# Kernel tuning notes

Hardware: AMD Instinct MI355X
Metric: run time of the kernel (lower is better)

Reference implementation:

```python
import jax, jax.numpy as jnp
from jax import lax
import numpy as np

NUM_LABELS = 48
BATCH, SEQ_LEN = 512, 1024


def setup_inputs() -> dict:
    key = jax.random.key(0)
    k1, k2, k3, k4, k5 = jax.random.split(key, 5)
    emissions = jax.random.normal(k1, (BATCH, SEQ_LEN, NUM_LABELS), dtype=jnp.float32)
    labels = jax.random.randint(k2, (BATCH, SEQ_LEN), 0, NUM_LABELS, dtype=jnp.int32)
    mask = jnp.ones((BATCH, SEQ_LEN), dtype=jnp.int32)
    transitions = jax.random.normal(k3, (NUM_LABELS, NUM_LABELS), dtype=jnp.float32)
    start_transitions = jax.random.normal(k4, (NUM_LABELS,), dtype=jnp.float32)
    end_transitions = jax.random.normal(k5, (NUM_LABELS,), dtype=jnp.float32)
    return {
        "emissions": emissions,
        "labels": labels,
        "mask": mask,
        "transitions": transitions,
        "start_transitions": start_transitions,
        "end_transitions": end_transitions,
    }


def _gold_score(emissions, labels, mask, transitions, start_transitions, end_transitions):
    maskf = mask.astype(emissions.dtype)
    # emissions gathered at gold labels: (B, T)
    emit = jnp.take_along_axis(emissions, labels[..., None], axis=2)[..., 0]
    # NOTE: original indexes transitions[labels_t, labels_{t-1}] (cur, prev)
    trans = transitions[labels[:, 1:], labels[:, :-1]]  # (B, T-1)
    lengths = jnp.sum(mask, axis=1) - 1  # index of last real token
    last_labels = jnp.take_along_axis(labels, lengths[:, None], axis=1)[:, 0]
    score = (start_transitions[labels[:, 0]] + emit[:, 0]
             + jnp.sum((emit[:, 1:] + trans) * maskf[:, 1:], axis=1)
             + end_transitions[last_labels])
    return score  # (B,)


def _forward_algorithm(emissions, mask, transitions, start_transitions, end_transitions):
    # carry: alpha scores (B, L)
    score0 = start_transitions[None, :] + emissions[:, 0]

    def step(score, xs):
        emit_t, mask_t = xs  # (B, L), (B,)
        # logsumexp over previous label i of score[b,i] + transitions[i,j]
        next_score = jax.nn.logsumexp(score[:, :, None] + transitions[None, :, :], axis=1) + emit_t
        score = jnp.where(mask_t[:, None].astype(bool), next_score, score)
        return score, None

    xs = (jnp.moveaxis(emissions[:, 1:], 1, 0), jnp.moveaxis(mask[:, 1:], 1, 0))
    score, _ = lax.scan(step, score0, xs)
    return jax.nn.logsumexp(score + end_transitions[None, :], axis=1)  # (B,)


def reference(emissions, labels, mask, transitions, start_transitions, end_transitions):
    gold = _gold_score(emissions, labels, mask, transitions, start_transitions, end_transitions)
    fwd = _forward_algorithm(emissions, mask, transitions, start_transitions, end_transitions)
    return jnp.mean(fwd - gold)
```

## Files before the change

kernel.cpp:

```cpp
#include <hip/hip_runtime.h>

constexpr int NL    = 48;
constexpr int SEQ   = 1024;
constexpr int BATCH = 512;

typedef float f2 __attribute__((ext_vector_type(2)));
typedef float f4 __attribute__((ext_vector_type(4)));

__device__ __forceinline__ f2 fma2(f2 a, f2 b, f2 c) {
    return __builtin_elementwise_fma(a, b, c);
}

#define CRF_STEP(T_, SLOT_, RN_) do {                                         \
    float ee_ = __expf(embuf[SLOT_]);                                         \
    int   mt_ = (int)((mb_cur >> (SLOT_)) & 1);                               \
    int   tn_ = (T_) + 8; if (tn_ > SEQ - 1) tn_ = SEQ - 1;                   \
    embuf[SLOT_] = em[tn_ * NL + jc];                                         \
    float rm_ = 1.0f;                                                         \
    if (RN_) {                                                                \
        float m_ = v;                                                         \
        _Pragma("unroll")                                                     \
        for (int o_ = 32; o_; o_ >>= 1) m_ = fmaxf(m_, __shfl_xor(m_, o_));   \
        rm_ = __builtin_amdgcn_rcpf(m_);                                      \
        S += __logf(m_);                                                      \
    }                                                                         \
    f2 c0_ = {0.f, 0.f}, c1_ = {0.f, 0.f};                                    \
    f2 c2_ = {0.f, 0.f}, c3_ = {0.f, 0.f};                                    \
    _Pragma("unroll")                                                         \
    for (int g_ = 0; g_ < 12; g_ += 2) {                                      \
        f4 s_ = svl4[g_];                                                     \
        c0_ = fma2(s_.xy, Ec2[2 * g_    ], c0_);                              \
        c1_ = fma2(s_.zw, Ec2[2 * g_ + 1], c1_);                              \
        f4 t_ = svl4[g_ + 1];                                                 \
        c2_ = fma2(t_.xy, Ec2[2 * g_ + 2], c2_);                              \
        c3_ = fma2(t_.zw, Ec2[2 * g_ + 3], c3_);                              \
    }                                                                         \
    f2 cs_ = (c0_ + c2_) + (c1_ + c3_);                                       \
    float acc_ = cs_.x + cs_.y;                                               \
    v = (mt_ ? acc_ * ee_ : v) * rm_;                                         \
    svl[tid] = v;                                                             \
} while (0)

__global__ __launch_bounds__(128)
__attribute__((amdgpu_waves_per_eu(1, 1)))
void crf_fused(
    const float* __restrict__ emissions, const int* __restrict__ labels,
    const int* __restrict__ mask, const float* __restrict__ trans,
    const float* __restrict__ startt, const float* __restrict__ endt,
    float* __restrict__ gold_out, float* __restrict__ fwd_out)
{
    const int b   = blockIdx.x;
    const int tid = threadIdx.x;
    const float* em = emissions + (size_t)b * SEQ * NL;
    const int*   mk = mask + b * SEQ;

    __shared__ alignas(16) float svl[64];

    if (tid < 64) {
        const int  j   = tid;
        const bool act = (j < NL);
        const int  jc  = act ? j : NL - 1;
        const f4*  svl4 = reinterpret_cast<const f4*>(svl);

        f2 Ec2[24];
        #pragma unroll
        for (int k = 0; k < 24; ++k) {
            f2 e_;
            e_.x = __expf(trans[(2 * k    ) * NL + jc]);
            e_.y = __expf(trans[(2 * k + 1) * NL + jc]);
            Ec2[k] = e_;
        }

        int mval = mk[tid & 7];
        unsigned long long mb_cur = __ballot(mval != 0);
        mval = mk[8 + (tid & 7)];

        float s0 = act ? (startt[jc] + em[jc]) : -3.0e38f;
        float m0 = s0;
        #pragma unroll
        for (int o = 32; o; o >>= 1) m0 = fmaxf(m0, __shfl_xor(m0, o));
        float v = act ? __expf(s0 - m0) : 0.0f;
        float S = m0;
        svl[tid] = v;

        float embuf[8];
        #pragma unroll
        for (int t = 1; t <= 8; ++t) embuf[t & 7] = em[t * NL + jc];

        CRF_STEP(1, 1, 0); CRF_STEP(2, 2, 0); CRF_STEP(3, 3, 0); CRF_STEP(4, 4, 0);
        CRF_STEP(5, 5, 1); CRF_STEP(6, 6, 0); CRF_STEP(7, 7, 0);

        for (int tb = 8; tb <= SEQ - 8; tb += 8) {
            mb_cur = __ballot(mval != 0);
            int tm = tb + 8 + (tid & 7);
            if (tm > SEQ - 1) tm = SEQ - 1;
            mval = mk[tm];
            CRF_STEP(tb + 0, 0, 1);
            CRF_STEP(tb + 1, 1, 0); CRF_STEP(tb + 2, 2, 0); CRF_STEP(tb + 3, 3, 0);
            CRF_STEP(tb + 4, 4, 1);
            CRF_STEP(tb + 5, 5, 0); CRF_STEP(tb + 6, 6, 0); CRF_STEP(tb + 7, 7, 0);
        }

        float w = act ? v * __expf(endt[jc]) : 0.0f;
        #pragma unroll
        for (int o = 32; o; o >>= 1) w += __shfl_xor(w, o);
        if (j == 0) fwd_out[b] = S + __logf(w);
    } else {
        const int l = tid - 64;
        const int* lb = labels + b * SEQ;

        float part = 0.0f; int mcnt = 0;
        for (int t = l; t < SEQ; t += 64) {
            int lt = lb[t];
            int mt = mk[t];
            mcnt += mt;
            if (t == 0) {
                part += startt[lt] + em[lt];
            } else {
                float e  = em[t * NL + lt];
                float tr = trans[lt * NL + lb[t - 1]];
                if (mt) part += e + tr;
            }
        }
        #pragma unroll
        for (int o = 32; o; o >>= 1) {
            part += __shfl_xor(part, o);
            mcnt += __shfl_xor(mcnt, o);
        }
        if (l == 0) {
            int len = mcnt - 1;
            gold_out[b] = part + endt[lb[len]];
        }
    }
}

__global__ __launch_bounds__(64) void crf_reduce(
    const float* __restrict__ gold, const float* __restrict__ fwd,
    float* __restrict__ out)
{
    const int l = threadIdx.x;
    float s = 0.0f;
    for (int bIdx = l; bIdx < BATCH; bIdx += 64) s += fwd[bIdx] - gold[bIdx];
    #pragma unroll
    for (int o = 32; o; o >>= 1) s += __shfl_xor(s, o);
    if (l == 0) out[0] = s * (1.0f / (float)BATCH);
}

extern "C" void kernel_launch(void* const* d_in, const int* in_sizes, int n_in,
                              void* d_out, int out_size, void* d_ws, size_t ws_size,
                              hipStream_t stream) {
    const float* emissions = (const float*)d_in[0];
    const int*   labels    = (const int*)d_in[1];
    const int*   mask      = (const int*)d_in[2];
    const float* trans     = (const float*)d_in[3];
    const float* startt    = (const float*)d_in[4];
    const float* endt      = (const float*)d_in[5];
    float*       out       = (float*)d_out;
    float*       wsf       = (float*)d_ws;

    crf_fused<<<BATCH, 128, 0, stream>>>(emissions, labels, mask, trans, startt, endt,
                                         wsf, wsf + BATCH);
    crf_reduce<<<1, 64, 0, stream>>>(wsf, wsf + BATCH, out);
}
```

Baseline: 324.0 us.

## Interleave two batch sequences per wave and compute renorm max from LDS

Each forward-recurrence wave now processes two batch elements in an interleaved fashion, so the independent dependency chains of two sequences can hide each other's LDS and FMA latency. Grid size is halved and each block gets two gold-score waves. The renormalisation max is now computed from the 48 values already loaded from shared memory, replacing a cross-lane shuffle reduction. The cost is doubled register pressure per wave and fewer blocks (256 on a device with many CUs), which may leave some compute units idle.

```diff
diff --git a/kernel.cpp b/kernel.cpp
--- a/kernel.cpp
+++ b/kernel.cpp
@@ -10,38 +10,51 @@
 __device__ __forceinline__ f2 fma2(f2 a, f2 b, f2 c) {
     return __builtin_elementwise_fma(a, b, c);
 }
-
-#define CRF_STEP(T_, SLOT_, RN_) do {                                         \
-    float ee_ = __expf(embuf[SLOT_]);                                         \
-    int   mt_ = (int)((mb_cur >> (SLOT_)) & 1);                               \
+__device__ __forceinline__ f2 max2(f2 a, f2 b) {
+    return __builtin_elementwise_max(a, b);
+}
+
+#define CRF_STEP(T_, SLOT_, RN_, v_, S_, eb_, mb_, em_, svl_, sv4_) do {      \
+    float ee_ = __expf(eb_[SLOT_]);                                           \
+    int   mt_ = (int)((mb_ >> (SLOT_)) & 1);                                  \
     int   tn_ = (T_) + 8; if (tn_ > SEQ - 1) tn_ = SEQ - 1;                   \
-    embuf[SLOT_] = em[tn_ * NL + jc];                                         \
-    float rm_ = 1.0f;                                                         \
-    if (RN_) {                                                                \
-        float m_ = v;                                                         \
-        _Pragma("unroll")                                                     \
-        for (int o_ = 32; o_; o_ >>= 1) m_ = fmaxf(m_, __shfl_xor(m_, o_));   \
-        rm_ = __builtin_amdgcn_rcpf(m_);                                      \
-        S += __logf(m_);                                                      \
-    }                                                                         \
+    eb_[SLOT_] = em_[tn_ * NL + jc];                                          \
+    f4 sv_[12];                                                               \
+    _Pragma("unroll")                                                         \
+    for (int g_ = 0; g_ < 12; ++g_) sv_[g_] = sv4_[g_];                       \
     f2 c0_ = {0.f, 0.f}, c1_ = {0.f, 0.f};                                    \
     f2 c2_ = {0.f, 0.f}, c3_ = {0.f, 0.f};                                    \
     _Pragma("unroll")                                                         \
     for (int g_ = 0; g_ < 12; g_ += 2) {                                      \
-        f4 s_ = svl4[g_];                                                     \
-        c0_ = fma2(s_.xy, Ec2[2 * g_    ], c0_);                              \
-        c1_ = fma2(s_.zw, Ec2[2 * g_ + 1], c1_);                              \
-        f4 t_ = svl4[g_ + 1];                                                 \
-        c2_ = fma2(t_.xy, Ec2[2 * g_ + 2], c2_);                              \
-        c3_ = fma2(t_.zw, Ec2[2 * g_ + 3], c3_);                              \
+        c0_ = fma2(sv_[g_    ].xy, Ec2[2 * g_    ], c0_);                     \
+        c1_ = fma2(sv_[g_    ].zw, Ec2[2 * g_ + 1], c1_);                     \
+        c2_ = fma2(sv_[g_ + 1].xy, Ec2[2 * g_ + 2], c2_);                     \
+        c3_ = fma2(sv_[g_ + 1].zw, Ec2[2 * g_ + 3], c3_);                     \
+    }                                                                         \
+    float rm_ = 1.0f;                                                         \
+    if (RN_) {                                                                \
+        f2 x0_ = max2(max2(sv_[0].xy,  sv_[0].zw),  max2(sv_[1].xy,  sv_[1].zw));  \
+        f2 x1_ = max2(max2(sv_[2].xy,  sv_[2].zw),  max2(sv_[3].xy,  sv_[3].zw));  \
+        f2 x2_ = max2(max2(sv_[4].xy,  sv_[4].zw),  max2(sv_[5].xy,  sv_[5].zw));  \
+        f2 x3_ = max2(max2(sv_[6].xy,  sv_[6].zw),  max2(sv_[7].xy,  sv_[7].zw));  \
+        f2 x4_ = max2(max2(sv_[8].xy,  sv_[8].zw),  max2(sv_[9].xy,  sv_[9].zw));  \
+        f2 x5_ = max2(max2(sv_[10].xy, sv_[10].zw), max2(sv_[11].xy, sv_[11].zw)); \
+        f2 y_  = max2(max2(x0_, x1_), max2(max2(x2_, x3_), max2(x4_, x5_)));  \
+        float m_ = fmaxf(y_.x, y_.y);                                         \
+        rm_ = __builtin_amdgcn_rcpf(m_);                                      \
+        S_ += __logf(m_);                                                     \
     }                                                                         \
     f2 cs_ = (c0_ + c2_) + (c1_ + c3_);                                       \
     float acc_ = cs_.x + cs_.y;                                               \
-    v = (mt_ ? acc_ * ee_ : v) * rm_;                                         \
-    svl[tid] = v;                                                             \
+    v_ = (mt_ ? acc_ * ee_ : v_) * rm_;                                       \
+    svl_[tid] = v_;                                                           \
 } while (0)
 
-__global__ __launch_bounds__(128)
+#define CRF_PAIR(T_, SLOT_, RN_)                                              \
+    CRF_STEP(T_, SLOT_, RN_, vA, SA, ebA, mbA, emA, svlA, sv4A);              \
+    CRF_STEP(T_, SLOT_, RN_, vB, SB, ebB, mbB, emB, svlB, sv4B)
+
+__global__ __launch_bounds__(192)
 __attribute__((amdgpu_waves_per_eu(1, 1)))
 void crf_fused(
     const float* __restrict__ emissions, const int* __restrict__ labels,
@@ -49,18 +62,26 @@
     const float* __restrict__ startt, const float* __restrict__ endt,
     float* __restrict__ gold_out, float* __restrict__ fwd_out)
 {
-    const int b   = blockIdx.x;
+    const int pb  = blockIdx.x;
     const int tid = threadIdx.x;
-    const float* em = emissions + (size_t)b * SEQ * NL;
-    const int*   mk = mask + b * SEQ;
-
-    __shared__ alignas(16) float svl[64];
+    const int bA  = 2 * pb;
+    const int bB  = 2 * pb + 1;
+
+    __shared__ alignas(16) float svl[2][64];
 
     if (tid < 64) {
         const int  j   = tid;
         const bool act = (j < NL);
         const int  jc  = act ? j : NL - 1;
-        const f4*  svl4 = reinterpret_cast<const f4*>(svl);
+
+        const float* emA = emissions + (size_t)bA * SEQ * NL;
+        const float* emB = emissions + (size_t)bB * SEQ * NL;
+        const int*   mkA = mask + bA * SEQ;
+        const int*   mkB = mask + bB * SEQ;
+        float* svlA = svl[0];
+        float* svlB = svl[1];
+        const f4* sv4A = reinterpret_cast<const f4*>(svlA);
+        const f4* sv4B = reinterpret_cast<const f4*>(svlB);
 
         f2 Ec2[24];
         #pragma unroll
@@ -71,53 +92,78 @@
             Ec2[k] = e_;
         }
 
-        int mval = mk[tid & 7];
-        unsigned long long mb_cur = __ballot(mval != 0);
-        mval = mk[8 + (tid & 7)];
-
-        float s0 = act ? (startt[jc] + em[jc]) : -3.0e38f;
-        float m0 = s0;
-        #pragma unroll
-        for (int o = 32; o; o >>= 1) m0 = fmaxf(m0, __shfl_xor(m0, o));
-        float v = act ? __expf(s0 - m0) : 0.0f;
-        float S = m0;
-        svl[tid] = v;
-
-        float embuf[8];
-        #pragma unroll
-        for (int t = 1; t <= 8; ++t) embuf[t & 7] = em[t * NL + jc];
-
-        CRF_STEP(1, 1, 0); CRF_STEP(2, 2, 0); CRF_STEP(3, 3, 0); CRF_STEP(4, 4, 0);
-        CRF_STEP(5, 5, 1); CRF_STEP(6, 6, 0); CRF_STEP(7, 7, 0);
+        int mvA = mkA[tid & 7];
+        int mvB = mkB[tid & 7];
+        unsigned long long mbA = __ballot(mvA != 0);
+        unsigned long long mbB = __ballot(mvB != 0);
+        mvA = mkA[8 + (tid & 7)];
+        mvB = mkB[8 + (tid & 7)];
+
+        float s0A = act ? (startt[jc] + emA[jc]) : -3.0e38f;
+        float s0B = act ? (startt[jc] + emB[jc]) : -3.0e38f;
+        float m0A = s0A, m0B = s0B;
+        #pragma unroll
+        for (int o = 32; o; o >>= 1) {
+            m0A = fmaxf(m0A, __shfl_xor(m0A, o));
+            m0B = fmaxf(m0B, __shfl_xor(m0B, o));
+        }
+        float vA = act ? __expf(s0A - m0A) : 0.0f;  float SA = m0A;
+        float vB = act ? __expf(s0B - m0B) : 0.0f;  float SB = m0B;
+        svlA[tid] = vA;
+        svlB[tid] = vB;
+
+        float ebA[8], ebB[8];
+        #pragma unroll
+        for (int t = 1; t <= 8; ++t) {
+            ebA[t & 7] = emA[t * NL + jc];
+            ebB[t & 7] = emB[t * NL + jc];
+        }
+
+        CRF_PAIR(1, 1, 0); CRF_PAIR(2, 2, 0); CRF_PAIR(3, 3, 0); CRF_PAIR(4, 4, 0);
+        CRF_PAIR(5, 5, 1); CRF_PAIR(6, 6, 0); CRF_PAIR(7, 7, 0);
 
         for (int tb = 8; tb <= SEQ - 8; tb += 8) {
-            mb_cur = __ballot(mval != 0);
+            mbA = __ballot(mvA != 0);
+            mbB = __ballot(mvB != 0);
             int tm = tb + 8 + (tid & 7);
             if (tm > SEQ - 1) tm = SEQ - 1;
-            mval = mk[tm];
-            CRF_STEP(tb + 0, 0, 1);
-            CRF_STEP(tb + 1, 1, 0); CRF_STEP(tb + 2, 2, 0); CRF_STEP(tb + 3, 3, 0);
-            CRF_STEP(tb + 4, 4, 1);
-            CRF_STEP(tb + 5, 5, 0); CRF_STEP(tb + 6, 6, 0); CRF_STEP(tb + 7, 7, 0);
-        }
-
-        float w = act ? v * __expf(endt[jc]) : 0.0f;
-        #pragma unroll
-        for (int o = 32; o; o >>= 1) w += __shfl_xor(w, o);
-        if (j == 0) fwd_out[b] = S + __logf(w);
+            mvA = mkA[tm];
+            mvB = mkB[tm];
+            CRF_PAIR(tb + 0, 0, 1);
+            CRF_PAIR(tb + 1, 1, 0); CRF_PAIR(tb + 2, 2, 0); CRF_PAIR(tb + 3, 3, 0);
+            CRF_PAIR(tb + 4, 4, 1);
+            CRF_PAIR(tb + 5, 5, 0); CRF_PAIR(tb + 6, 6, 0); CRF_PAIR(tb + 7, 7, 0);
+        }
+
+        float et = __expf(endt[jc]);
+        float wA = act ? vA * et : 0.0f;
+        float wB = act ? vB * et : 0.0f;
+        #pragma unroll
+        for (int o = 32; o; o >>= 1) {
+            wA += __shfl_xor(wA, o);
+            wB += __shfl_xor(wB, o);
+        }
+        if (j == 0) {
+            fwd_out[bA] = SA + __logf(wA);
+            fwd_out[bB] = SB + __logf(wB);
+        }
     } else {
-        const int l = tid - 64;
-        const int* lb = labels + b * SEQ;
+        const int  w   = (tid >> 6) - 1;
+        const int  l   = tid & 63;
+        const int  seq = 2 * pb + w;
+        const int* lb  = labels + seq * SEQ;
+        const int* mks = mask + seq * SEQ;
+        const float* ems = emissions + (size_t)seq * SEQ * NL;
 
         float part = 0.0f; int mcnt = 0;
         for (int t = l; t < SEQ; t += 64) {
             int lt = lb[t];
-            int mt = mk[t];
+            int mt = mks[t];
             mcnt += mt;
             if (t == 0) {
-                part += startt[lt] + em[lt];
+                part += startt[lt] + ems[lt];
             } else {
-                float e  = em[t * NL + lt];
+                float e  = ems[t * NL + lt];
                 float tr = trans[lt * NL + lb[t - 1]];
                 if (mt) part += e + tr;
             }
@@ -129,7 +175,7 @@
         }
         if (l == 0) {
             int len = mcnt - 1;
-            gold_out[b] = part + endt[lb[len]];
+            gold_out[seq] = part + endt[lb[len]];
         }
     }
 }
@@ -158,7 +204,7 @@
     float*       out       = (float*)d_out;
     float*       wsf       = (float*)d_ws;
 
-    crf_fused<<<BATCH, 128, 0, stream>>>(emissions, labels, mask, trans, startt, endt,
-                                         wsf, wsf + BATCH);
+    crf_fused<<<BATCH / 2, 192, 0, stream>>>(emissions, labels, mask, trans,
+                                             startt, endt, wsf, wsf + BATCH);
     crf_reduce<<<1, 64, 0, stream>>>(wsf, wsf + BATCH, out);
 }
```

Result: slower. 450.2 us (+39.0%).

## Replace LDS alpha broadcast with permlane swaps and DPP row rotates

Applied to the files above, without the earlier changes.

Each forward step now spreads the alpha vector across lanes with permlane32/permlane16 swaps and DPP row rotations instead of writing it to shared memory and reading it back. The transition exponentials are pre-permuted per lane to match the rotated operands. The max-renormalisation reduction also moves to DPP. This removes LDS round trips and their waits from the serial recurrence, at the cost of more cross-lane instructions and higher register pressure (64 coefficient registers).

```diff
diff --git a/kernel.cpp b/kernel.cpp
--- a/kernel.cpp
+++ b/kernel.cpp
@@ -4,41 +4,80 @@
 constexpr int SEQ   = 1024;
 constexpr int BATCH = 512;
 
-typedef float f2 __attribute__((ext_vector_type(2)));
-typedef float f4 __attribute__((ext_vector_type(4)));
-
-__device__ __forceinline__ f2 fma2(f2 a, f2 b, f2 c) {
-    return __builtin_elementwise_fma(a, b, c);
-}
+template<int N>
+__device__ __forceinline__ float rrf(float x) {
+    if constexpr (N == 0) return x;
+    else {
+        int xi = __float_as_int(x);
+        return __int_as_float(
+            __builtin_amdgcn_update_dpp(xi, xi, 0x120 | N, 0xF, 0xF, false));
+    }
+}
+template<int N>
+__device__ __forceinline__ unsigned rru(unsigned x) {
+    if constexpr (N == 0) return x;
+    else return (unsigned)
+        __builtin_amdgcn_update_dpp((int)x, (int)x, 0x120 | N, 0xF, 0xF, false);
+}
+
+__device__ __forceinline__ void spread4(unsigned x,
+        unsigned &c, unsigned &d, unsigned &e, unsigned &f) {
+    auto rA = __builtin_amdgcn_permlane32_swap(x, x, false, false);
+    auto rc = __builtin_amdgcn_permlane16_swap(rA[0], rA[0], false, false);
+    auto re = __builtin_amdgcn_permlane16_swap(rA[1], rA[1], false, false);
+    c = rc[0]; d = rc[1]; e = re[0]; f = re[1];
+}
+
+#define RF3(N_, pa_, pb_, pc_)                                                \
+    pa_ = fmaf(rrf<N_>(c_), EA[N_], pa_);                                     \
+    pb_ = fmaf(rrf<N_>(d_), EB[N_], pb_);                                     \
+    pc_ = fmaf(rrf<N_>(e_), EC[N_], pc_);
+#define RFF(N_, pd_) pd_ = fmaf(rrf<N_>(f_), ED[N_], pd_);
 
 #define CRF_STEP(T_, SLOT_, RN_) do {                                         \
     float ee_ = __expf(embuf[SLOT_]);                                         \
     int   mt_ = (int)((mb_cur >> (SLOT_)) & 1);                               \
     int   tn_ = (T_) + 8; if (tn_ > SEQ - 1) tn_ = SEQ - 1;                   \
     embuf[SLOT_] = em[tn_ * NL + jc];                                         \
+    unsigned cu_, du_, eu_, fu_;                                              \
+    spread4(__float_as_uint(v), cu_, du_, eu_, fu_);                          \
+    float c_ = __uint_as_float(cu_), d_ = __uint_as_float(du_);               \
+    float e_ = __uint_as_float(eu_), f_ = __uint_as_float(fu_);               \
     float rm_ = 1.0f;                                                         \
     if (RN_) {                                                                \
-        float m_ = v;                                                         \
-        _Pragma("unroll")                                                     \
-        for (int o_ = 32; o_; o_ >>= 1) m_ = fmaxf(m_, __shfl_xor(m_, o_));   \
-        rm_ = __builtin_amdgcn_rcpf(m_);                                      \
-        S += __logf(m_);                                                      \
+        float g_ = fmaxf(fmaxf(c_, d_), fmaxf(e_, f_));                       \
+        g_ = fmaxf(g_, rrf<8>(g_));  g_ = fmaxf(g_, rrf<4>(g_));              \
+        g_ = fmaxf(g_, rrf<2>(g_));  g_ = fmaxf(g_, rrf<1>(g_));              \
+        rm_ = __builtin_amdgcn_rcpf(g_);                                      \
+        S += __logf(g_);                                                      \
     }                                                                         \
-    f2 c0_ = {0.f, 0.f}, c1_ = {0.f, 0.f};                                    \
-    f2 c2_ = {0.f, 0.f}, c3_ = {0.f, 0.f};                                    \
-    _Pragma("unroll")                                                         \
-    for (int g_ = 0; g_ < 12; g_ += 2) {                                      \
-        f4 s_ = svl4[g_];                                                     \
-        c0_ = fma2(s_.xy, Ec2[2 * g_    ], c0_);                              \
-        c1_ = fma2(s_.zw, Ec2[2 * g_ + 1], c1_);                              \
-        f4 t_ = svl4[g_ + 1];                                                 \
-        c2_ = fma2(t_.xy, Ec2[2 * g_ + 2], c2_);                              \
-        c3_ = fma2(t_.zw, Ec2[2 * g_ + 3], c3_);                              \
+    float a0_ = 0.f, a1_ = 0.f, a2_ = 0.f;                                    \
+    float a3_ = 0.f, a4_ = 0.f, a5_ = 0.f;                                    \
+    RF3(0,  a0_, a1_, a2_)  RF3(1,  a3_, a4_, a5_)                            \
+    RF3(2,  a0_, a1_, a2_)  RF3(3,  a3_, a4_, a5_)                            \
+    RF3(4,  a0_, a1_, a2_)  RF3(5,  a3_, a4_, a5_)                            \
+    RF3(6,  a0_, a1_, a2_)  RF3(7,  a3_, a4_, a5_)                            \
+    RF3(8,  a0_, a1_, a2_)  RF3(9,  a3_, a4_, a5_)                            \
+    RF3(10, a0_, a1_, a2_)  RF3(11, a3_, a4_, a5_)                            \
+    RF3(12, a0_, a1_, a2_)  RF3(13, a3_, a4_, a5_)                            \
+    RF3(14, a0_, a1_, a2_)  RF3(15, a3_, a4_, a5_)                            \
+    if (useF) {         \
+        RFF(0,  a0_) RFF(1,  a1_) RFF(2,  a2_) RFF(3,  a3_)                   \
+        RFF(4,  a4_) RFF(5,  a5_) RFF(6,  a0_) RFF(7,  a1_)                   \
+        RFF(8,  a2_) RFF(9,  a3_) RFF(10, a4_) RFF(11, a5_)                   \
+        RFF(12, a0_) RFF(13, a1_) RFF(14, a2_) RFF(15, a3_)                   \
     }                                                                         \
-    f2 cs_ = (c0_ + c2_) + (c1_ + c3_);                                       \
-    float acc_ = cs_.x + cs_.y;                                               \
+    float acc_ = ((a0_ + a3_) + (a1_ + a4_)) + (a2_ + a5_);                   \
     v = (mt_ ? acc_ * ee_ : v) * rm_;                                         \
-    svl[tid] = v;                                                             \
+} while (0)
+
+#define EPREP(N_) do {                                                        \
+    unsigned i0 = rru<N_>(ic_), i1 = rru<N_>(id_);                            \
+    unsigned i2 = rru<N_>(ie_), i3 = rru<N_>(if_);                            \
+    EA[N_] = (i0 < (unsigned)NL) ? __expf(trans[i0 * NL + jc]) : 0.0f;        \
+    EB[N_] = (i1 < (unsigned)NL) ? __expf(trans[i1 * NL + jc]) : 0.0f;        \
+    EC[N_] = (i2 < (unsigned)NL) ? __expf(trans[i2 * NL + jc]) : 0.0f;        \
+    ED[N_] = (i3 < (unsigned)NL) ? __expf(trans[i3 * NL + jc]) : 0.0f;        \
 } while (0)
 
 __global__ __launch_bounds__(128)
@@ -54,22 +93,20 @@
     const float* em = emissions + (size_t)b * SEQ * NL;
     const int*   mk = mask + b * SEQ;
 
-    __shared__ alignas(16) float svl[64];
-
     if (tid < 64) {
         const int  j   = tid;
         const bool act = (j < NL);
         const int  jc  = act ? j : NL - 1;
-        const f4*  svl4 = reinterpret_cast<const f4*>(svl);
-
-        f2 Ec2[24];
-        #pragma unroll
-        for (int k = 0; k < 24; ++k) {
-            f2 e_;
-            e_.x = __expf(trans[(2 * k    ) * NL + jc]);
-            e_.y = __expf(trans[(2 * k + 1) * NL + jc]);
-            Ec2[k] = e_;
-        }
+
+        unsigned ic_, id_, ie_, if_;
+        spread4((unsigned)j, ic_, id_, ie_, if_);
+        const bool useF = (__ballot(if_ < (unsigned)NL) != 0ull);
+
+        float EA[16], EB[16], EC[16], ED[16];
+        EPREP(0);  EPREP(1);  EPREP(2);  EPREP(3);
+        EPREP(4);  EPREP(5);  EPREP(6);  EPREP(7);
+        EPREP(8);  EPREP(9);  EPREP(10); EPREP(11);
+        EPREP(12); EPREP(13); EPREP(14); EPREP(15);
 
         int mval = mk[tid & 7];
         unsigned long long mb_cur = __ballot(mval != 0);
@@ -81,7 +118,6 @@
         for (int o = 32; o; o >>= 1) m0 = fmaxf(m0, __shfl_xor(m0, o));
         float v = act ? __expf(s0 - m0) : 0.0f;
         float S = m0;
-        svl[tid] = v;
 
         float embuf[8];
         #pragma unroll
```

After: 453.5 us. 40.0% more time.
